# Performance work log

Hardware: AMD Instinct MI355X
Metric: run time of the kernel (lower is better)

The kernel has to match this reference:

```python
import jax, jax.numpy as jnp
import numpy as np

EPS = 1e-6
GROUPS = 32


def group_norm(x, scale, bias):
    # x: [b, c, d, h, w]
    b, c, d, h, w = x.shape
    xg = x.reshape(b, GROUPS, c // GROUPS, d, h, w)
    mean = xg.mean(axis=(2, 3, 4, 5), keepdims=True)
    var = xg.var(axis=(2, 3, 4, 5), keepdims=True)
    xn = ((xg - mean) * jax.lax.rsqrt(var + EPS)).reshape(b, c, d, h, w)
    return xn * scale[None, :, None, None, None] + bias[None, :, None, None, None]


def setup_inputs() -> dict:
    key = jax.random.key(0)
    ks = jax.random.split(key, 6)
    C = 512
    x = jax.random.normal(ks[0], (2, C, 16, 16, 16), dtype=jnp.float32)
    s = 1.0 / np.sqrt(C)
    return {
        "x": x,
        "gn_scale": jnp.ones((C,), jnp.float32),
        "gn_bias": jnp.zeros((C,), jnp.float32),
        "wq": jax.random.normal(ks[1], (C, C), jnp.float32) * s,
        "bq": jnp.zeros((C,), jnp.float32),
        "wk": jax.random.normal(ks[2], (C, C), jnp.float32) * s,
        "bk": jnp.zeros((C,), jnp.float32),
        "wv": jax.random.normal(ks[3], (C, C), jnp.float32) * s,
        "bv": jnp.zeros((C,), jnp.float32),
        "wproj": jax.random.normal(ks[4], (C, C), jnp.float32) * s,
        "bproj": jnp.zeros((C,), jnp.float32),
    }


def reference(x, gn_scale, gn_bias, wq, bq, wk, bk, wv, bv, wproj, bproj):
    b, c, d, h, w = x.shape
    h_ = group_norm(x, gn_scale, gn_bias)
    hf = h_.reshape(b, c, d * h * w)  # [b, c, N]
    # 1x1x1 convs == per-position channel matmuls
    q = jnp.einsum("oc,bcn->bon", wq, hf) + bq[None, :, None]
    k = jnp.einsum("oc,bcn->bon", wk, hf) + bk[None, :, None]
    v = jnp.einsum("oc,bcn->bon", wv, hf) + bv[None, :, None]
    # attn[b, i, j] = softmax_j(q_i . k_j / sqrt(c))
    attn = jnp.einsum("bci,bcj->bij", q, k) * (c ** -0.5)
    attn = jax.nn.softmax(attn, axis=-1)
    # out[b, c, i] = sum_j v[b, c, j] * attn[b, i, j]
    out = jnp.einsum("bcj,bij->bci", v, attn)
    out = jnp.einsum("oc,bcn->bon", wproj, out) + bproj[None, :, None]
    return x + out.reshape(b, c, d, h, w)
```

## Files before the change

kernel.cpp:

```cpp
#include <hip/hip_runtime.h>
#include <hip/hip_bf16.h>

#define BB 2
#define CC 512
#define GG 32
#define NN 4096
#define EPSV 1e-6f

typedef __attribute__((ext_vector_type(4))) float f32x4;
typedef __attribute__((ext_vector_type(8))) short s16x8;
typedef __attribute__((ext_vector_type(4))) short s16x4;

__device__ __forceinline__ ushort f2bf(float f){
  union { float f; unsigned u; } v; v.f = f;
  unsigned r = v.u + 0x7fffu + ((v.u >> 16) & 1u);
  return (ushort)(r >> 16);
}
__device__ __forceinline__ short f2bfs(float f){ return (short)f2bf(f); }
__device__ __forceinline__ float b2f(ushort u){
  union { unsigned u; float f; } v; v.u = ((unsigned)u) << 16; return v.f;
}

__device__ __forceinline__ f32x4 mfma16(s16x8 a, s16x8 b, f32x4 c){
  return __builtin_amdgcn_mfma_f32_16x16x32_bf16(a, b, c, 0, 0, 0);
}

#define GLOAD_LDS16(g, l) __builtin_amdgcn_global_load_lds( \
    (const __attribute__((address_space(1))) void*)(g),     \
    (__attribute__((address_space(3))) void*)(l), 16, 0, 0)

__global__ __launch_bounds__(256) void k_convert_w(const float* __restrict__ wq, const float* __restrict__ wk,
                                                   const float* __restrict__ wv, const float* __restrict__ wp,
                                                   ushort* __restrict__ wbf){
  int idx = blockIdx.x * 256 + threadIdx.x;
  const float* srcs[4] = {wq, wk, wv, wp};
  #pragma unroll
  for (int m = 0; m < 4; m++){
    float4 v = reinterpret_cast<const float4*>(srcs[m])[idx];
    ushort4 o; o.x = f2bf(v.x); o.y = f2bf(v.y); o.z = f2bf(v.z); o.w = f2bf(v.w);
    reinterpret_cast<ushort4*>(wbf + (size_t)m * CC * CC)[idx] = o;
  }
}

__global__ __launch_bounds__(256) void k_gn_stats(const float* __restrict__ x, float* __restrict__ stats){
  int bg = blockIdx.x;
  const float* p = x + (size_t)bg * (16 * NN);
  float s = 0.f, ss = 0.f;
  for (int i = threadIdx.x; i < 16 * NN / 4; i += 256){
    float4 v = reinterpret_cast<const float4*>(p)[i];
    s  += v.x + v.y + v.z + v.w;
    ss += v.x*v.x + v.y*v.y + v.z*v.z + v.w*v.w;
  }
  #pragma unroll
  for (int off = 32; off; off >>= 1){ s += __shfl_down(s, off); ss += __shfl_down(ss, off); }
  __shared__ float rs_[4], rss_[4];
  int w = threadIdx.x >> 6, lane = threadIdx.x & 63;
  if (lane == 0){ rs_[w] = s; rss_[w] = ss; }
  __syncthreads();
  if (threadIdx.x == 0){
    float S = rs_[0] + rs_[1] + rs_[2] + rs_[3];
    float SS = rss_[0] + rss_[1] + rss_[2] + rss_[3];
    float inv = 1.0f / (16.0f * NN);
    float mean = S * inv;
    float var = SS * inv - mean * mean;
    stats[bg * 2 + 0] = mean;
    stats[bg * 2 + 1] = rsqrtf(var + EPSV);
  }
}

__global__ __launch_bounds__(256) void k_gn_apply(const float* __restrict__ x, const float* __restrict__ gsc,
                                                  const float* __restrict__ gbi, const float* __restrict__ stats,
                                                  ushort* __restrict__ hf){
  __shared__ ushort tr[32][520];
  int b = blockIdx.y;
  int nb = blockIdx.x * 32;
  int t = threadIdx.x;
  int n = t & 31, cr = t >> 5;
  const float* xb = x + (size_t)b * CC * NN;
  for (int c0 = 0; c0 < CC; c0 += 8){
    int c = c0 + cr;
    float mean = stats[(b * GG + (c >> 4)) * 2 + 0];
    float rstd = stats[(b * GG + (c >> 4)) * 2 + 1];
    float v = xb[(size_t)c * NN + nb + n];
    tr[n][c] = f2bf((v - mean) * rstd * gsc[c] + gbi[c]);
  }
  __syncthreads();
  ushort* out = hf + ((size_t)b * NN + nb) * CC;
  int c8 = (t & 63) * 8;
  int nrow0 = t >> 6;
  #pragma unroll
  for (int i = 0; i < 8; i++){
    int nr = nrow0 + i * 4;
    *reinterpret_cast<s16x8*>(&out[(size_t)nr * CC + c8]) =
      *reinterpret_cast<const s16x8*>(&tr[nr][c8]);
  }
}

__global__ __launch_bounds__(256) void k_gemm_qkv(const ushort* __restrict__ W, const ushort* __restrict__ Bt,
                                                  const float* __restrict__ bq, const float* __restrict__ bk,
                                                  const float* __restrict__ bv,
                                                  ushort* __restrict__ qo, ushort* __restrict__ ko,
                                                  ushort* __restrict__ vo, float rs){
  __shared__ ushort Al[3][64][72];
  __shared__ ushort Bl[64][72];
  __shared__ float bl[3][64];
  int b = blockIdx.z, ob = blockIdx.y * 64, nb = blockIdx.x * 64;
  int t = threadIdx.x, w = t >> 6, l = t & 63;
  int lr = l & 15, lk = l >> 4;
  int wo = (w >> 1) * 32, wn = (w & 1) * 32;
  if (t < 64){ bl[0][t] = bq[ob + t]; bl[1][t] = bk[ob + t]; bl[2][t] = bv[ob + t]; }
  const ushort* Bp = Bt + ((size_t)b * NN + nb) * CC;
  int srow = t >> 2, scol = (t & 3) * 16;
  f32x4 acc[3][2][2] = {};
  for (int k0 = 0; k0 < CC; k0 += 64){
    #pragma unroll
    for (int m = 0; m < 3; m++){
      const ushort* Ap = W + (size_t)m * CC * CC + (size_t)ob * CC;
      *reinterpret_cast<s16x8*>(&Al[m][srow][scol])     = *reinterpret_cast<const s16x8*>(&Ap[(size_t)srow * CC + k0 + scol]);
      *reinterpret_cast<s16x8*>(&Al[m][srow][scol + 8]) = *reinterpret_cast<const s16x8*>(&Ap[(size_t)srow * CC + k0 + scol + 8]);
    }
    *reinterpret_cast<s16x8*>(&Bl[srow][scol])     = *reinterpret_cast<const s16x8*>(&Bp[(size_t)srow * CC + k0 + scol]);
    *reinterpret_cast<s16x8*>(&Bl[srow][scol + 8]) = *reinterpret_cast<const s16x8*>(&Bp[(size_t)srow * CC + k0 + scol + 8]);
    __syncthreads();
    #pragma unroll
    for (int kk = 0; kk < 2; kk++){
      s16x8 b0 = *reinterpret_cast<const s16x8*>(&Bl[wn + lr][kk * 32 + lk * 8]);
      s16x8 b1 = *reinterpret_cast<const s16x8*>(&Bl[wn + 16 + lr][kk * 32 + lk * 8]);
      #pragma unroll
      for (int m = 0; m < 3; m++){
        s16x8 a0 = *reinterpret_cast<const s16x8*>(&Al[m][wo + lr][kk * 32 + lk * 8]);
        s16x8 a1 = *reinterpret_cast<const s16x8*>(&Al[m][wo + 16 + lr][kk * 32 + lk * 8]);
        acc[m][0][0] = mfma16(a0, b0, acc[m][0][0]);
        acc[m][0][1] = mfma16(a0, b1, acc[m][0][1]);
        acc[m][1][0] = mfma16(a1, b0, acc[m][1][0]);
        acc[m][1][1] = mfma16(a1, b1, acc[m][1][1]);
      }
    }
    __syncthreads();
  }
  #pragma unroll
  for (int m = 0; m < 2; m++){
    ushort* dst = (m == 0) ? qo : ko;
    float scl = (m == 0) ? rs : 1.0f;
    #pragma unroll
    for (int oi = 0; oi < 2; oi++)
      #pragma unroll
      for (int nj = 0; nj < 2; nj++){
        int o0 = wo + oi * 16 + lk * 4;
        int n  = nb + wn + nj * 16 + lr;
        s16x4 pv;
        #pragma unroll
        for (int r = 0; r < 4; r++) pv[r] = f2bfs((acc[m][oi][nj][r] + bl[m][o0 + r]) * scl);
        *reinterpret_cast<s16x4*>(&dst[((size_t)b * NN + n) * CC + ob + o0]) = pv;
      }
  }
  #pragma unroll
  for (int oi = 0; oi < 2; oi++)
    #pragma unroll
    for (int nj = 0; nj < 2; nj++){
      int o0 = wo + oi * 16 + lk * 4;
      int ncl = wn + nj * 16 + lr;
      #pragma unroll
      for (int r = 0; r < 4; r++) Al[0][o0 + r][ncl] = f2bf(acc[2][oi][nj][r] + bl[2][o0 + r]);
    }
  __syncthreads();
  {
    int o = t >> 2, ns = (t & 3) * 16;
    ushort* dst = &vo[((size_t)b * CC + ob + o) * NN + nb + ns];
    *reinterpret_cast<s16x8*>(dst)     = *reinterpret_cast<const s16x8*>(&Al[0][o][ns]);
    *reinterpret_cast<s16x8*>(dst + 8) = *reinterpret_cast<const s16x8*>(&Al[0][o][ns + 8]);
  }
}

__global__ __launch_bounds__(256) void k_gemm_s(const ushort* __restrict__ qt, const ushort* __restrict__ kt,
                                                ushort* __restrict__ P, float* __restrict__ part){
  __shared__ __align__(16) char smem[35840];
  ushort* Ks = (ushort*)smem;
  ushort* Qs = (ushort*)(smem + 16384);
  int lin = blockIdx.x + 32 * blockIdx.y + 1024 * blockIdx.z;
  int tt0 = (lin & 7) * 256 + (lin >> 3);
  int jblk = tt0 & 31;
  int pair = tt0 >> 5;
  int b = pair >> 5;
  int j0 = jblk * 128, i0 = (pair & 31) * 128;
  int t = threadIdx.x, w = t >> 6, l = t & 63;
  int lr = l & 15, lk = l >> 4;
  int wj = (w >> 1) * 64, wi = (w & 1) * 64;
  const ushort* kb = kt + ((size_t)b * NN + j0) * CC;
  const ushort* qb = qt + ((size_t)b * NN + i0) * CC;
  int srow = l >> 3;
  int schunk = (l & 7) ^ srow;
  f32x4 acc[4][4] = {};
  for (int k0 = 0; k0 < CC; k0 += 64){
    __syncthreads();
    #pragma unroll
    for (int tt = 0; tt < 8; tt++){
      int inst = w * 8 + tt;
      if (inst < 16){
        const ushort* src = kb + (size_t)(inst * 8 + srow) * CC + k0 + schunk * 8;
        GLOAD_LDS16(src, Ks + inst * 512);
      } else {
        int q = inst - 16;
        const ushort* src = qb + (size_t)(q * 8 + srow) * CC + k0 + schunk * 8;
        GLOAD_LDS16(src, Qs + q * 512);
      }
    }
    __syncthreads();
    #pragma unroll
    for (int kk = 0; kk < 2; kk++){
      int xs = ((kk * 4 + lk) ^ (lr & 7)) * 8;
      s16x8 af[4], bf[4];
      #pragma unroll
      for (int s = 0; s < 4; s++){
        af[s] = *(const s16x8*)&Ks[(wj + s * 16 + lr) * 64 + xs];
        bf[s] = *(const s16x8*)&Qs[(wi + s * 16 + lr) * 64 + xs];
      }
      #pragma unroll
      for (int sj = 0; sj < 4; sj++)
        #pragma unroll
        for (int si = 0; si < 4; si++)
          acc[sj][si] = mfma16(af[sj], bf[si], acc[sj][si]);
    }
  }
  __syncthreads();
  ushort* Pe = (ushort*)smem;
  float rsum[4] = {0.f, 0.f, 0.f, 0.f};
  #pragma unroll
  for (int sj = 0; sj < 4; sj++)
    #pragma unroll
    for (int si = 0; si < 4; si++){
      int il = wi + si * 16 + lr;
      int jl = wj + sj * 16 + lk * 4;
      s16x4 pk;
      #pragma unroll
      for (int r = 0; r < 4; r++){
        float e = exp2f(acc[sj][si][r]);
        pk[r] = f2bfs(e);
        rsum[si] += e;
      }
      *(s16x4*)&Pe[il * 136 + jl] = pk;
    }
  #pragma unroll
  for (int si = 0; si < 4; si++){
    float s = rsum[si];
    s += __shfl_xor(s, 16);
    s += __shfl_xor(s, 32);
    if (lk == 0){
      int il = wi + si * 16 + lr;
      part[((size_t)b * NN + i0 + il) * 64 + jblk * 2 + (w >> 1)] = s;
    }
  }
  __syncthreads();
  {
    int row = t >> 1, cs = (t & 1) * 64;
    ushort* dst = P + ((size_t)b * NN + i0 + row) * NN + j0 + cs;
    #pragma unroll
    for (int k = 0; k < 8; k++)
      *(s16x8*)&dst[k * 8] = *(const s16x8*)&Pe[row * 136 + cs + k * 8];
  }
}

__global__ __launch_bounds__(256) void k_rowsum2(const float* __restrict__ part, float* __restrict__ linv){
  int row = blockIdx.x * 4 + (threadIdx.x >> 6);
  int l = threadIdx.x & 63;
  float s = part[(size_t)row * 64 + l];
  #pragma unroll
  for (int off = 32; off; off >>= 1) s += __shfl_down(s, off);
  if (l == 0) linv[row] = 1.0f / s;
}

__global__ __launch_bounds__(512) void k_gemm_o(const ushort* __restrict__ P, const ushort* __restrict__ vv,
                                                const float* __restrict__ linv, ushort* __restrict__ ot){
  __shared__ __align__(16) char smem[24576];
  ushort* Vs = (ushort*)smem;
  ushort* Ps = (ushort*)(smem + 8192);
  int lin = blockIdx.x + 8 * blockIdx.y + 256 * blockIdx.z;
  int tt0 = (lin & 7) * 64 + (lin >> 3);
  int cblk = tt0 & 7;
  int pair = tt0 >> 3;
  int b = pair >> 5;
  int c0 = cblk * 64, i0 = (pair & 31) * 128;
  int t = threadIdx.x, w = t >> 6, l = t & 63;
  int lr = l & 15, lk = l >> 4;
  int wi = (w >> 1) * 32, wc = (w & 1) * 32;
  const ushort* vb = vv + ((size_t)b * CC + c0) * NN;
  const ushort* pb = P + ((size_t)b * NN + i0) * NN;
  int srow = l >> 3;
  int schunk = (l & 7) ^ srow;
  f32x4 acc[2][2] = {};
  for (int k0 = 0; k0 < NN; k0 += 64){
    __syncthreads();
    #pragma unroll
    for (int tt = 0; tt < 3; tt++){
      int inst = w * 3 + tt;
      if (inst < 8){
        const ushort* src = vb + (size_t)(inst * 8 + srow) * NN + k0 + schunk * 8;
        GLOAD_LDS16(src, Vs + inst * 512);
      } else {
        int q = inst - 8;
        const ushort* src = pb + (size_t)(q * 8 + srow) * NN + k0 + schunk * 8;
        GLOAD_LDS16(src, Ps + q * 512);
      }
    }
    __syncthreads();
    #pragma unroll
    for (int kk = 0; kk < 2; kk++){
      int xs = ((kk * 4 + lk) ^ (lr & 7)) * 8;
      s16x8 af[2], bf[2];
      af[0] = *(const s16x8*)&Vs[(wc + lr) * 64 + xs];
      af[1] = *(const s16x8*)&Vs[(wc + 16 + lr) * 64 + xs];
      bf[0] = *(const s16x8*)&Ps[(wi + lr) * 64 + xs];
      bf[1] = *(const s16x8*)&Ps[(wi + 16 + lr) * 64 + xs];
      acc[0][0] = mfma16(af[0], bf[0], acc[0][0]);
      acc[0][1] = mfma16(af[0], bf[1], acc[0][1]);
      acc[1][0] = mfma16(af[1], bf[0], acc[1][0]);
      acc[1][1] = mfma16(af[1], bf[1], acc[1][1]);
    }
  }
  __syncthreads();
  ushort* Oe = (ushort*)smem;
  #pragma unroll
  for (int si = 0; si < 2; si++){
    int il = wi + si * 16 + lr;
    float li = linv[(size_t)b * NN + i0 + il];
    #pragma unroll
    for (int sc = 0; sc < 2; sc++){
      int cl = wc + sc * 16 + lk * 4;
      s16x4 pk;
      #pragma unroll
      for (int r = 0; r < 4; r++) pk[r] = f2bfs(acc[sc][si][r] * li);
      *(s16x4*)&Oe[il * 72 + cl] = pk;
    }
  }
  __syncthreads();
  {
    int row = t >> 2, cs = (t & 3) * 16;
    ushort* dst = ot + ((size_t)b * NN + i0 + row) * CC + c0 + cs;
    #pragma unroll
    for (int k = 0; k < 2; k++)
      *(s16x8*)&dst[k * 8] = *(const s16x8*)&Oe[row * 72 + cs + k * 8];
  }
}

__global__ __launch_bounds__(256) void k_gemm_proj(const ushort* __restrict__ A, const ushort* __restrict__ Bt,
                                                   const float* __restrict__ bias, float* __restrict__ o32,
                                                   const float* __restrict__ xres){
  __shared__ ushort Al[64][72];
  __shared__ ushort Bl[64][72];
  __shared__ float bl[64];
  __shared__ float trf[64 * 68];
  int b = blockIdx.z, ob = blockIdx.y * 64, nb = blockIdx.x * 64;
  int t = threadIdx.x, w = t >> 6, l = t & 63;
  int lr = l & 15, lk = l >> 4;
  int wo = (w >> 1) * 32, wn = (w & 1) * 32;
  if (t < 64) bl[t] = bias[ob + t];
  const ushort* Bp = Bt + ((size_t)b * NN + nb) * CC;
  const ushort* Ap = A + (size_t)ob * CC;
  int srow = t >> 2, scol = (t & 3) * 16;
  f32x4 acc[2][2] = {};
  for (int k0 = 0; k0 < CC; k0 += 64){
    *reinterpret_cast<s16x8*>(&Al[srow][scol])     = *reinterpret_cast<const s16x8*>(&Ap[(size_t)srow * CC + k0 + scol]);
    *reinterpret_cast<s16x8*>(&Al[srow][scol + 8]) = *reinterpret_cast<const s16x8*>(&Ap[(size_t)srow * CC + k0 + scol + 8]);
    *reinterpret_cast<s16x8*>(&Bl[srow][scol])     = *reinterpret_cast<const s16x8*>(&Bp[(size_t)srow * CC + k0 + scol]);
    *reinterpret_cast<s16x8*>(&Bl[srow][scol + 8]) = *reinterpret_cast<const s16x8*>(&Bp[(size_t)srow * CC + k0 + scol + 8]);
    __syncthreads();
    #pragma unroll
    for (int kk = 0; kk < 2; kk++){
      s16x8 a0 = *reinterpret_cast<const s16x8*>(&Al[wo + lr][kk * 32 + lk * 8]);
      s16x8 a1 = *reinterpret_cast<const s16x8*>(&Al[wo + 16 + lr][kk * 32 + lk * 8]);
      s16x8 b0 = *reinterpret_cast<const s16x8*>(&Bl[wn + lr][kk * 32 + lk * 8]);
      s16x8 b1 = *reinterpret_cast<const s16x8*>(&Bl[wn + 16 + lr][kk * 32 + lk * 8]);
      acc[0][0] = mfma16(a0, b0, acc[0][0]);
      acc[0][1] = mfma16(a0, b1, acc[0][1]);
      acc[1][0] = mfma16(a1, b0, acc[1][0]);
      acc[1][1] = mfma16(a1, b1, acc[1][1]);
    }
    __syncthreads();
  }
  #pragma unroll
  for (int oi = 0; oi < 2; oi++)
    #pragma unroll
    for (int nj = 0; nj < 2; nj++){
      int o0 = wo + oi * 16 + lk * 4;
      int ncl = wn + nj * 16 + lr;
      #pragma unroll
      for (int r = 0; r < 4; r++) trf[(o0 + r) * 68 + ncl] = acc[oi][nj][r] + bl[o0 + r];
    }
  __syncthreads();
  {
    int o = t >> 2, ns = (t & 3) * 16;
    size_t base = ((size_t)b * CC + ob + o) * NN + nb + ns;
    #pragma unroll
    for (int q = 0; q < 4; q++){
      float4 xv = *reinterpret_cast<const float4*>(&xres[base + q * 4]);
      float4 ov;
      ov.x = xv.x + trf[o * 68 + ns + q * 4 + 0];
      ov.y = xv.y + trf[o * 68 + ns + q * 4 + 1];
      ov.z = xv.z + trf[o * 68 + ns + q * 4 + 2];
      ov.w = xv.w + trf[o * 68 + ns + q * 4 + 3];
      *reinterpret_cast<float4*>(&o32[base + q * 4]) = ov;
    }
  }
}

extern "C" void kernel_launch(void* const* d_in, const int* in_sizes, int n_in,
                              void* d_out, int out_size, void* d_ws, size_t ws_size,
                              hipStream_t stream){
  const float* x   = (const float*)d_in[0];
  const float* gsc = (const float*)d_in[1];
  const float* gbi = (const float*)d_in[2];
  const float* wq  = (const float*)d_in[3];
  const float* bq  = (const float*)d_in[4];
  const float* wk  = (const float*)d_in[5];
  const float* bk  = (const float*)d_in[6];
  const float* wv  = (const float*)d_in[7];
  const float* bv  = (const float*)d_in[8];
  const float* wp  = (const float*)d_in[9];
  const float* bp  = (const float*)d_in[10];
  char* ws = (char*)d_ws;
  const size_t MB = 1024 * 1024;
  ushort* wbf  = (ushort*)ws;
  ushort* qtb  = (ushort*)(ws + 2 * MB);
  ushort* ktb  = (ushort*)(ws + 10 * MB);
  ushort* vvb  = (ushort*)(ws + 18 * MB);
  ushort* hfb  = (ushort*)(ws + 26 * MB);
  ushort* Pbuf = (ushort*)(ws + 34 * MB);
  float* linv  = (float*)(ws + 98 * MB);
  float* stats = (float*)(ws + 98 * MB + 64 * 1024);
  float* part  = (float*)(ws + 26 * MB);
  ushort* otb = hfb;

  const float rs = 0.044194173824159216f * 1.4426950408889634f;

  k_convert_w<<<256, 256, 0, stream>>>(wq, wk, wv, wp, wbf);
  k_gn_stats<<<64, 256, 0, stream>>>(x, stats);
  k_gn_apply<<<dim3(128, 2, 1), 256, 0, stream>>>(x, gsc, gbi, stats, hfb);
  k_gemm_qkv<<<dim3(64, 8, 2), 256, 0, stream>>>(wbf, hfb, bq, bk, bv, qtb, ktb, vvb, rs);
  k_gemm_s<<<dim3(32, 32, 2), 256, 0, stream>>>(qtb, ktb, Pbuf, part);
  k_rowsum2<<<2048, 256, 0, stream>>>(part, linv);
  k_gemm_o<<<dim3(8, 32, 2), 512, 0, stream>>>(Pbuf, vvb, linv, otb);
  k_gemm_proj<<<dim3(64, 8, 2), 256, 0, stream>>>(wbf + 3 * CC * CC, otb, bp, (float*)d_out, x);
}
```

Baseline: 202.0 us.

## Double-buffer LDS tiles in score and output GEMM kernels

Both attention GEMM kernels (QK^T scores and P·V) now use two LDS buffers. The next K-slice is issued with global-to-LDS loads while the current slice feeds the MFMAs, and the loop drops to one barrier per iteration instead of two. The aim is to hide global load latency behind matrix math. The cost is doubled LDS per block (64KB and 48KB), which can lower how many blocks fit on a CU.

```diff
diff --git a/kernel.cpp b/kernel.cpp
--- a/kernel.cpp
+++ b/kernel.cpp
@@ -174,9 +174,7 @@
 
 __global__ __launch_bounds__(256) void k_gemm_s(const ushort* __restrict__ qt, const ushort* __restrict__ kt,
                                                 ushort* __restrict__ P, float* __restrict__ part){
-  __shared__ __align__(16) char smem[35840];
-  ushort* Ks = (ushort*)smem;
-  ushort* Qs = (ushort*)(smem + 16384);
+  __shared__ __align__(16) char smem[65536];
   int lin = blockIdx.x + 32 * blockIdx.y + 1024 * blockIdx.z;
   int tt0 = (lin & 7) * 256 + (lin >> 3);
   int jblk = tt0 & 31;
@@ -190,22 +188,32 @@
   const ushort* qb = qt + ((size_t)b * NN + i0) * CC;
   int srow = l >> 3;
   int schunk = (l & 7) ^ srow;
+
+#define STAGE_S(BUF, K0)                                                          \
+  {                                                                               \
+    ushort* Ks_ = (ushort*)(smem + (BUF) * 16384);                                \
+    ushort* Qs_ = (ushort*)(smem + 32768 + (BUF) * 16384);                        \
+    _Pragma("unroll")                                                             \
+    for (int tt = 0; tt < 8; tt++){                                               \
+      int inst = w * 8 + tt;                                                      \
+      if (inst < 16){                                                             \
+        const ushort* src = kb + (size_t)(inst * 8 + srow) * CC + (K0) + schunk * 8; \
+        GLOAD_LDS16(src, Ks_ + inst * 512);                                       \
+      } else {                                                                    \
+        int q = inst - 16;                                                        \
+        const ushort* src = qb + (size_t)(q * 8 + srow) * CC + (K0) + schunk * 8; \
+        GLOAD_LDS16(src, Qs_ + q * 512);                                          \
+      }                                                                           \
+    }                                                                             \
+  }
+
   f32x4 acc[4][4] = {};
-  for (int k0 = 0; k0 < CC; k0 += 64){
-    __syncthreads();
-    #pragma unroll
-    for (int tt = 0; tt < 8; tt++){
-      int inst = w * 8 + tt;
-      if (inst < 16){
-        const ushort* src = kb + (size_t)(inst * 8 + srow) * CC + k0 + schunk * 8;
-        GLOAD_LDS16(src, Ks + inst * 512);
-      } else {
-        int q = inst - 16;
-        const ushort* src = qb + (size_t)(q * 8 + srow) * CC + k0 + schunk * 8;
-        GLOAD_LDS16(src, Qs + q * 512);
-      }
-    }
-    __syncthreads();
+  STAGE_S(0, 0)
+  __syncthreads();
+  for (int s8 = 0; s8 < 8; s8++){
+    if (s8 < 7) STAGE_S((s8 + 1) & 1, (s8 + 1) * 64)
+    const ushort* Ks = (const ushort*)(smem + (s8 & 1) * 16384);
+    const ushort* Qs = (const ushort*)(smem + 32768 + (s8 & 1) * 16384);
     #pragma unroll
     for (int kk = 0; kk < 2; kk++){
       int xs = ((kk * 4 + lk) ^ (lr & 7)) * 8;
@@ -221,8 +229,9 @@
         for (int si = 0; si < 4; si++)
           acc[sj][si] = mfma16(af[sj], bf[si], acc[sj][si]);
     }
-  }
-  __syncthreads();
+    __syncthreads();
+  }
+#undef STAGE_S
   ushort* Pe = (ushort*)smem;
   float rsum[4] = {0.f, 0.f, 0.f, 0.f};
   #pragma unroll
@@ -271,9 +280,7 @@
 
 __global__ __launch_bounds__(512) void k_gemm_o(const ushort* __restrict__ P, const ushort* __restrict__ vv,
                                                 const float* __restrict__ linv, ushort* __restrict__ ot){
-  __shared__ __align__(16) char smem[24576];
-  ushort* Vs = (ushort*)smem;
-  ushort* Ps = (ushort*)(smem + 8192);
+  __shared__ __align__(16) char smem[49152];
   int lin = blockIdx.x + 8 * blockIdx.y + 256 * blockIdx.z;
   int tt0 = (lin & 7) * 64 + (lin >> 3);
   int cblk = tt0 & 7;
@@ -287,22 +294,32 @@
   const ushort* pb = P + ((size_t)b * NN + i0) * NN;
   int srow = l >> 3;
   int schunk = (l & 7) ^ srow;
+
+#define STAGE_O(BUF, K0)                                                          \
+  {                                                                               \
+    ushort* Vs_ = (ushort*)(smem + (BUF) * 8192);                                 \
+    ushort* Ps_ = (ushort*)(smem + 16384 + (BUF) * 16384);                        \
+    _Pragma("unroll")                                                             \
+    for (int tt = 0; tt < 3; tt++){                                               \
+      int inst = w * 3 + tt;                                                      \
+      if (inst < 8){                                                              \
+        const ushort* src = vb + (size_t)(inst * 8 + srow) * NN + (K0) + schunk * 8; \
+        GLOAD_LDS16(src, Vs_ + inst * 512);                                       \
+      } else {                                                                    \
+        int q = inst - 8;                                                         \
+        const ushort* src = pb + (size_t)(q * 8 + srow) * NN + (K0) + schunk * 8; \
+        GLOAD_LDS16(src, Ps_ + q * 512);                                          \
+      }                                                                           \
+    }                                                                             \
+  }
+
   f32x4 acc[2][2] = {};
-  for (int k0 = 0; k0 < NN; k0 += 64){
-    __syncthreads();
-    #pragma unroll
-    for (int tt = 0; tt < 3; tt++){
-      int inst = w * 3 + tt;
-      if (inst < 8){
-        const ushort* src = vb + (size_t)(inst * 8 + srow) * NN + k0 + schunk * 8;
-        GLOAD_LDS16(src, Vs + inst * 512);
-      } else {
-        int q = inst - 8;
-        const ushort* src = pb + (size_t)(q * 8 + srow) * NN + k0 + schunk * 8;
-        GLOAD_LDS16(src, Ps + q * 512);
-      }
-    }
-    __syncthreads();
+  STAGE_O(0, 0)
+  __syncthreads();
+  for (int s64 = 0; s64 < 64; s64++){
+    if (s64 < 63) STAGE_O((s64 + 1) & 1, (s64 + 1) * 64)
+    const ushort* Vs = (const ushort*)(smem + (s64 & 1) * 8192);
+    const ushort* Ps = (const ushort*)(smem + 16384 + (s64 & 1) * 16384);
     #pragma unroll
     for (int kk = 0; kk < 2; kk++){
       int xs = ((kk * 4 + lk) ^ (lr & 7)) * 8;
@@ -316,8 +333,9 @@
       acc[1][0] = mfma16(af[1], bf[0], acc[1][0]);
       acc[1][1] = mfma16(af[1], bf[1], acc[1][1]);
     }
-  }
-  __syncthreads();
+    __syncthreads();
+  }
+#undef STAGE_O
   ushort* Oe = (ushort*)smem;
   #pragma unroll
   for (int si = 0; si < 2; si++){
```

Result: faster. 194.0 us (-3.9%).
